# Performance work log

Measured on AMD Instinct MI355X. Metric: run time of the kernel, lower is better.

The kernel has to match this reference:

```python
import jax, jax.numpy as jnp
import numpy as np

OFFSET = 1e-6   # undefined global in source; small positive stabilizer
COS_EPS = 1e-8  # F.cosine_similarity default eps

B, N, M = 128, 2048, 128


def setup_inputs() -> dict:
    key = jax.random.key(0)
    ks = jax.random.split(key, 9)
    return {
        "memory": jax.random.normal(ks[0], (B, N, M), jnp.float32),
        "k_t": jax.random.normal(ks[1], (B, M), jnp.float32),
        "beta_t": jax.random.uniform(ks[2], (B,), jnp.float32),
        "g_t": jax.random.uniform(ks[3], (B,), jnp.float32),
        "w_t_minus_1": jax.random.uniform(ks[4], (B, N), jnp.float32),
        "s_t": jax.random.uniform(ks[5], (B, 3), jnp.float32),
        "gamma_t": jax.random.uniform(ks[6], (B,), jnp.float32),
        "e_t": jax.random.uniform(ks[7], (B, M), jnp.float32),
        "a_t": jax.random.normal(ks[8], (B, M), jnp.float32),
    }


def reference(memory, k_t, beta_t, g_t, w_t_minus_1, s_t, gamma_t, e_t, a_t):
    # ---- content_addressing (faithful to source, incl. w_tilde_t = w_{t-1} quirk) ----
    mk = memory + OFFSET                     # [B,N,M]
    kk = k_t[:, None, :] + OFFSET            # [B,1,M]
    dot = jnp.sum(mk * kk, axis=-1)          # [B,N]
    nm = jnp.maximum(jnp.sqrt(jnp.sum(mk * mk, -1)), COS_EPS)            # [B,N]
    nk = jnp.maximum(jnp.sqrt(jnp.sum(kk * kk, -1)), COS_EPS)            # [B,1]
    K = dot / (nm * nk)                      # cosine similarity, [B,N]
    w_c = jax.nn.softmax(beta_t[:, None] * K, axis=1)                    # [B,N]
    w_g = g_t[:, None] * w_c + (1.0 - g_t[:, None]) * w_t_minus_1        # [B,N]
    w_pow = w_t_minus_1 ** gamma_t[:, None]                              # sharpening on w_{t-1}
    w_t = jnp.sum(w_pow, axis=1, keepdims=True) + OFFSET                 # [B,1]
    w_t = jnp.broadcast_to(w_t, w_t_minus_1.shape)                       # [B,N] (source .repeat)

    # ---- writing: rank-1 erase/add memory update ----
    erase = w_t[:, :, None] * e_t[:, None, :]                            # [B,N,M]
    M_new = memory * (1.0 - erase) + w_t[:, :, None] * a_t[:, None, :]   # [B,N,M]

    # ---- reading ----
    r_t = jnp.einsum('bn,bnm->bm', w_t, M_new)                           # [B,M]

    # single concatenated output so every chain stays live: [B, M + 2N]
    return jnp.concatenate([r_t, w_t, w_g], axis=1)
```

## Files before the change

kernel.cpp:

```cpp
#include <hip/hip_runtime.h>
#include <hip/hip_bf16.h>
#include <math.h>

#define BB 128
#define NN 2048
#define MM 128
#define ROWS_PER_BLOCK 128
#define CHUNKS (NN / ROWS_PER_BLOCK)
#define OFFSET_EPS 1e-6f
#define COS_EPS 1e-8f

__global__ __launch_bounds__(256) void pass_a(
    const float* __restrict__ memory, const float* __restrict__ k_t,
    const float* __restrict__ beta_t, float* __restrict__ colsum_part,
    float* __restrict__ score)
{
    const int b     = blockIdx.x / CHUNKS;
    const int chunk = blockIdx.x % CHUNKS;
    const int r0    = chunk * ROWS_PER_BLOCK;
    const int wave  = threadIdx.x >> 6;
    const int lane  = threadIdx.x & 63;
    const int half  = lane >> 5;
    const int l32   = lane & 31;

    float4 kv = *(const float4*)(k_t + b * MM + 4 * l32);
    const float k0 = kv.x + OFFSET_EPS, k1 = kv.y + OFFSET_EPS,
                k2 = kv.z + OFFSET_EPS, k3 = kv.w + OFFSET_EPS;

    float nks = k0 * k0 + k1 * k1 + k2 * k2 + k3 * k3;
    #pragma unroll
    for (int s = 16; s; s >>= 1) nks += __shfl_xor(nks, s);
    const float nk = fmaxf(sqrtf(nks), COS_EPS);
    const float beta_over_nk = beta_t[b] / nk;

    const float* mbase = memory + (size_t)b * NN * MM;
    float cs0 = 0.f, cs1 = 0.f, cs2 = 0.f, cs3 = 0.f;

    #pragma unroll 4
    for (int i = 0; i < ROWS_PER_BLOCK / 8; ++i) {
        const int n = r0 + 8 * i + 2 * wave + half;
        float4 mv = *(const float4*)(mbase + (size_t)n * MM + 4 * l32);
        cs0 += mv.x; cs1 += mv.y; cs2 += mv.z; cs3 += mv.w;
        const float v0 = mv.x + OFFSET_EPS, v1 = mv.y + OFFSET_EPS,
                    v2 = mv.z + OFFSET_EPS, v3 = mv.w + OFFSET_EPS;
        float dot = v0 * k0 + v1 * k1 + v2 * k2 + v3 * k3;
        float sq  = v0 * v0 + v1 * v1 + v2 * v2 + v3 * v3;
        #pragma unroll
        for (int s = 16; s; s >>= 1) {
            dot += __shfl_xor(dot, s);
            sq  += __shfl_xor(sq,  s);
        }
        if (l32 == 0) {
            const float nm = fmaxf(sqrtf(sq), COS_EPS);
            score[b * NN + n] = dot * beta_over_nk / nm;
        }
    }

    __shared__ float s_col[8][MM];
    const int hw = wave * 2 + half;
    s_col[hw][4 * l32 + 0] = cs0;
    s_col[hw][4 * l32 + 1] = cs1;
    s_col[hw][4 * l32 + 2] = cs2;
    s_col[hw][4 * l32 + 3] = cs3;
    __syncthreads();
    if (threadIdx.x < MM) {
        float v = 0.f;
        #pragma unroll
        for (int j = 0; j < 8; ++j) v += s_col[j][threadIdx.x];
        colsum_part[(size_t)chunk * BB * MM + b * MM + threadIdx.x] = v;
    }
}

__global__ __launch_bounds__(256) void pass_b(
    const float* __restrict__ score,  const float* __restrict__ g_t,
    const float* __restrict__ w_prev, const float* __restrict__ gamma_t,
    const float* __restrict__ e_t,    const float* __restrict__ a_t,
    const float* __restrict__ colsum_part, float* __restrict__ out)
{
    const int b   = blockIdx.x;
    const int tid = threadIdx.x;
    __shared__ float red[256];

    float sc[8];
    float mx = -INFINITY;
    #pragma unroll
    for (int i = 0; i < 8; ++i) {
        sc[i] = score[b * NN + tid + 256 * i];
        mx = fmaxf(mx, sc[i]);
    }
    red[tid] = mx; __syncthreads();
    for (int s = 128; s; s >>= 1) {
        if (tid < s) red[tid] = fmaxf(red[tid], red[tid + s]);
        __syncthreads();
    }
    mx = red[0]; __syncthreads();

    float sum = 0.f;
    #pragma unroll
    for (int i = 0; i < 8; ++i) {
        sc[i] = __expf(sc[i] - mx);
        sum += sc[i];
    }
    red[tid] = sum; __syncthreads();
    for (int s = 128; s; s >>= 1) {
        if (tid < s) red[tid] += red[tid + s];
        __syncthreads();
    }
    const float inv_sum = 1.f / red[0];
    __syncthreads();

    const float g     = g_t[b];
    const float gamma = gamma_t[b];
    float wg[8];
    float psum = 0.f;
    #pragma unroll
    for (int i = 0; i < 8; ++i) {
        const float w = w_prev[b * NN + tid + 256 * i];
        wg[i] = g * (sc[i] * inv_sum) + (1.f - g) * w;
        psum += __powf(w, gamma);
    }
    red[tid] = psum; __syncthreads();
    for (int s = 128; s; s >>= 1) {
        if (tid < s) red[tid] += red[tid + s];
        __syncthreads();
    }
    const float S = red[0] + OFFSET_EPS;

    float* orow = out + (size_t)b * (MM + 2 * NN);
    #pragma unroll
    for (int i = 0; i < 8; ++i) {
        const int n = tid + 256 * i;
        orow[MM + n]      = S;
        orow[MM + NN + n] = wg[i];
    }
    if (tid < MM) {
        float cs = 0.f;
        #pragma unroll
        for (int c = 0; c < CHUNKS; ++c)
            cs += colsum_part[(size_t)c * BB * MM + b * MM + tid];
        const float r = S * ((1.f - S * e_t[b * MM + tid]) * cs +
                             (float)NN * S * a_t[b * MM + tid]);
        orow[tid] = r;
    }
}

extern "C" void kernel_launch(void* const* d_in, const int* in_sizes, int n_in,
                              void* d_out, int out_size, void* d_ws, size_t ws_size,
                              hipStream_t stream) {
    const float* memory  = (const float*)d_in[0];
    const float* k_t     = (const float*)d_in[1];
    const float* beta_t  = (const float*)d_in[2];
    const float* g_t     = (const float*)d_in[3];
    const float* w_prev  = (const float*)d_in[4];
    const float* gamma_t = (const float*)d_in[6];
    const float* e_t     = (const float*)d_in[7];
    const float* a_t     = (const float*)d_in[8];
    float* out = (float*)d_out;

    float* colsum_part = (float*)d_ws;
    float* score       = colsum_part + CHUNKS * BB * MM;

    const int grid_a = BB * CHUNKS;
    pass_a<<<grid_a, 256, 0, stream>>>(memory, k_t, beta_t, colsum_part, score);
    pass_b<<<BB, 256, 0, stream>>>(score, g_t, w_prev, gamma_t, e_t, a_t,
                                   colsum_part, out);
}
```

Measured before the change: 214.7 us.

## Stage memory rows in padded LDS tile and compute row dots from shared memory

pass_a now loads each block's 128x128 memory tile into padded shared memory with coalesced float4 loads, taking column sums along the way. Each row's dot product and squared norm are then computed by two threads reading from LDS, so the per-row 5-step shuffle reductions become a single shuffle. The OFFSET term is factored out algebraically using precomputed k sums and row sums. The cost is about 68KB of LDS per block, which limits occupancy, plus an extra barrier.

```diff
diff --git a/kernel.cpp b/kernel.cpp
--- a/kernel.cpp
+++ b/kernel.cpp
@@ -5,8 +5,9 @@
 #define BB 128
 #define NN 2048
 #define MM 128
-#define ROWS_PER_BLOCK 128
-#define CHUNKS (NN / ROWS_PER_BLOCK)
+#define ROWS 128
+#define CHUNKS (NN / ROWS)
+#define STRIDE (MM + 4)
 #define OFFSET_EPS 1e-6f
 #define COS_EPS 1e-8f
 
@@ -15,59 +16,77 @@
     const float* __restrict__ beta_t, float* __restrict__ colsum_part,
     float* __restrict__ score)
 {
+    __shared__ float tile[ROWS * STRIDE];
+    __shared__ float ks[MM];
+    __shared__ float s_col[8][MM];
+    __shared__ float s_bon;
+    __shared__ float s_epsK1;
+
     const int b     = blockIdx.x / CHUNKS;
     const int chunk = blockIdx.x % CHUNKS;
-    const int r0    = chunk * ROWS_PER_BLOCK;
-    const int wave  = threadIdx.x >> 6;
-    const int lane  = threadIdx.x & 63;
-    const int half  = lane >> 5;
-    const int l32   = lane & 31;
+    const int r0    = chunk * ROWS;
+    const int t     = threadIdx.x;
 
-    float4 kv = *(const float4*)(k_t + b * MM + 4 * l32);
-    const float k0 = kv.x + OFFSET_EPS, k1 = kv.y + OFFSET_EPS,
-                k2 = kv.z + OFFSET_EPS, k3 = kv.w + OFFSET_EPS;
-
-    float nks = k0 * k0 + k1 * k1 + k2 * k2 + k3 * k3;
-    #pragma unroll
-    for (int s = 16; s; s >>= 1) nks += __shfl_xor(nks, s);
-    const float nk = fmaxf(sqrtf(nks), COS_EPS);
-    const float beta_over_nk = beta_t[b] / nk;
-
-    const float* mbase = memory + (size_t)b * NN * MM;
-    float cs0 = 0.f, cs1 = 0.f, cs2 = 0.f, cs3 = 0.f;
-
-    #pragma unroll 4
-    for (int i = 0; i < ROWS_PER_BLOCK / 8; ++i) {
-        const int n = r0 + 8 * i + 2 * wave + half;
-        float4 mv = *(const float4*)(mbase + (size_t)n * MM + 4 * l32);
-        cs0 += mv.x; cs1 += mv.y; cs2 += mv.z; cs3 += mv.w;
-        const float v0 = mv.x + OFFSET_EPS, v1 = mv.y + OFFSET_EPS,
-                    v2 = mv.z + OFFSET_EPS, v3 = mv.w + OFFSET_EPS;
-        float dot = v0 * k0 + v1 * k1 + v2 * k2 + v3 * k3;
-        float sq  = v0 * v0 + v1 * v1 + v2 * v2 + v3 * v3;
+    if (t < 32) {
+        float4 kv = *(const float4*)(k_t + b * MM + 4 * t);
+        const float e0 = kv.x + OFFSET_EPS, e1 = kv.y + OFFSET_EPS,
+                    e2 = kv.z + OFFSET_EPS, e3 = kv.w + OFFSET_EPS;
+        *(float4*)&ks[4 * t] = make_float4(e0, e1, e2, e3);
+        float s2 = e0 * e0 + e1 * e1 + e2 * e2 + e3 * e3;
+        float s1 = e0 + e1 + e2 + e3;
         #pragma unroll
         for (int s = 16; s; s >>= 1) {
-            dot += __shfl_xor(dot, s);
-            sq  += __shfl_xor(sq,  s);
+            s2 += __shfl_xor(s2, s);
+            s1 += __shfl_xor(s1, s);
         }
-        if (l32 == 0) {
-            const float nm = fmaxf(sqrtf(sq), COS_EPS);
-            score[b * NN + n] = dot * beta_over_nk / nm;
+        if (t == 0) {
+            s_bon   = beta_t[b] / fmaxf(sqrtf(s2), COS_EPS);
+            s_epsK1 = OFFSET_EPS * s1;
         }
     }
 
-    __shared__ float s_col[8][MM];
-    const int hw = wave * 2 + half;
-    s_col[hw][4 * l32 + 0] = cs0;
-    s_col[hw][4 * l32 + 1] = cs1;
-    s_col[hw][4 * l32 + 2] = cs2;
-    s_col[hw][4 * l32 + 3] = cs3;
+    const float* src = memory + (size_t)(b * NN + r0) * MM;
+    float cs0 = 0.f, cs1 = 0.f, cs2 = 0.f, cs3 = 0.f;
+    #pragma unroll
+    for (int i = 0; i < 16; ++i) {
+        float4 v = *(const float4*)(src + i * 1024 + 4 * t);
+        cs0 += v.x; cs1 += v.y; cs2 += v.z; cs3 += v.w;
+        const int row = i * 8 + (t >> 5);
+        const int col = (4 * t) & 127;
+        *(float4*)&tile[row * STRIDE + col] = v;
+    }
+    *(float4*)&s_col[t >> 5][(4 * t) & 127] = make_float4(cs0, cs1, cs2, cs3);
     __syncthreads();
-    if (threadIdx.x < MM) {
+
+    const int r = t >> 1;
+    const int h = t & 1;
+    const float* vrow = &tile[r * STRIDE + h * 64];
+    const float* krow = &ks[h * 64];
+    float dot = 0.f, sq = 0.f, rs = 0.f;
+    #pragma unroll
+    for (int j = 0; j < 16; ++j) {
+        float4 v = *(const float4*)(vrow + 4 * j);
+        float4 k = *(const float4*)(krow + 4 * j);
+        dot += v.x * k.x + v.y * k.y + v.z * k.z + v.w * k.w;
+        sq  += v.x * v.x + v.y * v.y + v.z * v.z + v.w * v.w;
+        rs  += v.x + v.y + v.z + v.w;
+    }
+    dot += __shfl_xor(dot, 1);
+    sq  += __shfl_xor(sq, 1);
+    rs  += __shfl_xor(rs, 1);
+    if (h == 0) {
+        const float d   = dot + s_epsK1;
+        const float nm2 = sq + 2.0f * OFFSET_EPS * rs
+                          + (float)MM * OFFSET_EPS * OFFSET_EPS;
+        const float nm  = fmaxf(sqrtf(nm2), COS_EPS);
+        score[b * NN + r0 + r] = d * s_bon / nm;
+    }
+
+    if (t < MM) {
         float v = 0.f;
         #pragma unroll
-        for (int j = 0; j < 8; ++j) v += s_col[j][threadIdx.x];
-        colsum_part[(size_t)chunk * BB * MM + b * MM + threadIdx.x] = v;
+        for (int g = 0; g < 8; ++g) v += s_col[g][t];
+        colsum_part[(size_t)chunk * (BB * MM) + b * MM + t] = v;
     }
 }
 
@@ -137,7 +156,7 @@
         float cs = 0.f;
         #pragma unroll
         for (int c = 0; c < CHUNKS; ++c)
-            cs += colsum_part[(size_t)c * BB * MM + b * MM + tid];
+            cs += colsum_part[(size_t)c * (BB * MM) + b * MM + tid];
         const float r = S * ((1.f - S * e_t[b * MM + tid]) * cs +
                              (float)NN * S * a_t[b * MM + tid]);
         orow[tid] = r;
```

Result: no change. 213.2 us (-0.7%).
